# Performance work log

Hardware: AMD Instinct MI355X
Metric: run time of the kernel (lower is better)

## Reference

```python
import jax, jax.numpy as jnp
import numpy as np

NEG_SLOPE = 0.01  # torch F.leaky_relu default


def _gat_stack(x, W, a1w, a1b, a2w, a2b):
    """One GAT stack over all heads.
    x: (B, N, F_in); W: (H, F_in, d); a1w/a2w: (H, d); a1b/a2b: (H,)
    returns (B, N, H*d) -- heads concatenated in order along last dim.
    """
    # 1x1 conv1d (no bias) == per-node linear projection
    fts = jnp.einsum('bnf,hfd->hbnd', x, W)                      # (H,B,N,d)
    f1 = jnp.einsum('hbnd,hd->hbn', fts, a1w) + a1b[:, None, None]
    f2 = jnp.einsum('hbnd,hd->hbn', fts, a2w) + a2b[:, None, None]
    # logits[h,b,i,j] = f1[h,b,i] + f2[h,b,j]  (f_1.permute + f_2 broadcast)
    logits = f1[:, :, :, None] + f2[:, :, None, :]               # (H,B,N,N)
    coefs = jax.nn.softmax(jax.nn.leaky_relu(logits, NEG_SLOPE), axis=-1)
    vals = jnp.einsum('hbnm,hbmd->hbnd', coefs, fts)             # bmm aggregation
    ret = jax.nn.elu(vals + fts)                                 # residual-within-head + ELU activation
    B, N = x.shape[0], x.shape[1]
    return jnp.transpose(ret, (1, 2, 0, 3)).reshape(B, N, -1)    # cat(heads, dim=-1)


def setup_inputs() -> dict:
    key = jax.random.key(0)
    ks = jax.random.split(key, 7)
    B, N, F_in, H, d = 32, 512, 128, 8, 64
    hidden = H * d  # 512
    s = 0.05
    return {
        'x':   jax.random.normal(ks[0], (B, N, F_in), jnp.float32),
        'W0':  jax.random.normal(ks[1], (H, F_in, d), jnp.float32) * s,
        'W1':  jax.random.normal(ks[2], (H, hidden, d), jnp.float32) * s,
        'a1w': jax.random.normal(ks[3], (2, H, d), jnp.float32) * s,
        'a1b': jax.random.normal(ks[4], (2, H), jnp.float32) * s,
        'a2w': jax.random.normal(ks[5], (2, H, d), jnp.float32) * s,
        'a2b': jax.random.normal(ks[6], (2, H), jnp.float32) * s,
    }


def reference(x, W0, W1, a1w, a1b, a2w, a2b):
    # stack 0: input dim = num_random_sample
    h = _gat_stack(x, W0, a1w[0], a1b[0], a2w[0], a2b[0])
    # stack 1: input dim = hidden_dim
    out = _gat_stack(h, W1, a1w[1], a1b[1], a2w[1], a2b[1])
    return out
```

## Files before the change

### kernel.cpp

```cpp
#include <hip/hip_runtime.h>
#include <hip/hip_bf16.h>
#include <stdint.h>

typedef __attribute__((ext_vector_type(8))) short short8;
typedef __attribute__((ext_vector_type(4))) float f32x4;

#define L2E 1.44269504f
#define FN  131072

__device__ __forceinline__ short f2bf(float f) {
    unsigned u = __builtin_bit_cast(unsigned, f);
    return (short)((u + 0x8000u) >> 16);
}
__device__ __forceinline__ short f2bf_rn(float f) {
    __hip_bfloat16 h = __float2bfloat16(f);
    return __builtin_bit_cast(short, h);
}
__device__ __forceinline__ float bf2f(short s) {
    unsigned u = ((unsigned)(unsigned short)s) << 16;
    return __builtin_bit_cast(float, u);
}

__device__ __forceinline__ void gld16(void* l, const void* g) {
    __builtin_amdgcn_global_load_lds(
        (const __attribute__((address_space(1))) unsigned*)g,
        (__attribute__((address_space(3))) unsigned*)l, 16, 0, 0);
}

#define PIPE_OPEN()  do { __builtin_amdgcn_s_barrier();                        \
                          __builtin_amdgcn_sched_barrier(0);                   \
                          asm volatile("" ::: "memory"); } while (0)
#define PIPE_CLOSE() do { asm volatile("s_waitcnt lgkmcnt(0)" ::: "memory");   \
                          __builtin_amdgcn_sched_barrier(0);                   \
                          __builtin_amdgcn_s_barrier(); } while (0)

__global__ void wtrans_kernel(const float* __restrict__ W0, const float* __restrict__ W1,
                              short* __restrict__ BT0, short* __restrict__ BT1) {
    int idx = blockIdx.x * 256 + threadIdx.x;
    if (idx < 8 * 128 * 64) {
        int h = idx >> 13;
        int k = (idx >> 6) & 127;
        int dd = idx & 63;
        BT0[(h * 64 + dd) * 128 + k] = f2bf(W0[idx]);
    } else {
        int j = idx - 8 * 128 * 64;
        int h = j >> 15;
        int k = (j >> 6) & 511;
        int dd = j & 63;
        BT1[(h * 64 + dd) * 512 + k] = f2bf(W1[j]);
    }
}

template <typename AT>
__global__ __launch_bounds__(256, 2)
void gemm_kernel(const AT* __restrict__ A, const short* __restrict__ BT,
                 short* __restrict__ fts, int K,
                 const float* __restrict__ a1w, const float* __restrict__ a1b,
                 const float* __restrict__ a2w, const float* __restrict__ a2b,
                 float* __restrict__ fbuf) {
    __shared__ __align__(16) short As[2][128 * 64];
    __shared__ __align__(16) short Bs[2][128 * 64];

    const int tid  = threadIdx.x;
    const int lane = tid & 63;
    const int w    = tid >> 6;
    const int wr   = w >> 1, wc = w & 1;
    const int quad = lane >> 4, l15 = lane & 15;

    const int id = blockIdx.x;
    const int bx = (id >> 3) & 3;
    const int by = ((id >> 5) << 3) + (id & 7);
    const int m0 = by * 128;
    const int n0 = bx * 128;

    const int rl   = lane >> 3;
    const int cpos = lane & 7;
    const int kcl  = cpos ^ rl;

    f32x4 acc[4][4];
    for (int i = 0; i < 4; ++i)
        for (int j = 0; j < 4; ++j) { f32x4 z = {0.f, 0.f, 0.f, 0.f}; acc[i][j] = z; }

    const int nkb = K >> 6;

    if constexpr (sizeof(AT) == 4) {
        for (int kb = 0; kb < nkb; ++kb) {
            __syncthreads();
            for (int i = 0; i < 8; ++i) {
                int id2 = tid + i * 256;
                int row = id2 >> 4, q = id2 & 15;
                int c = q >> 1, half = q & 1;
                float4 v = *(const float4*)((const float*)A + (size_t)(m0 + row) * K + kb * 64 + q * 4);
                ushort4 p;
                p.x = (unsigned short)f2bf(v.x);
                p.y = (unsigned short)f2bf(v.y);
                p.z = (unsigned short)f2bf(v.z);
                p.w = (unsigned short)f2bf(v.w);
                int swz = c ^ (row & 7);
                *(ushort4*)(As[0] + row * 64 + swz * 8 + half * 4) = p;
            }
            for (int i = 0; i < 4; ++i) {
                int rowb = w * 32 + i * 8;
                gld16(Bs[0] + rowb * 64,
                      BT + (size_t)(n0 + rowb + rl) * K + kb * 64 + kcl * 8);
            }
            __syncthreads();
            short8 af[2][4], bf[2][4];
            for (int ks = 0; ks < 2; ++ks) {
                for (int mf = 0; mf < 4; ++mf) {
                    int row = wr * 64 + mf * 16 + l15;
                    af[ks][mf] = *(const short8*)(As[0] + row * 64 + (((ks * 4 + quad) ^ (row & 7)) << 3));
                }
                for (int nf = 0; nf < 4; ++nf) {
                    int row = wc * 64 + nf * 16 + l15;
                    bf[ks][nf] = *(const short8*)(Bs[0] + row * 64 + (((ks * 4 + quad) ^ (row & 7)) << 3));
                }
            }
            for (int ks = 0; ks < 2; ++ks)
                for (int mf = 0; mf < 4; ++mf)
                    for (int nf = 0; nf < 4; ++nf)
                        acc[mf][nf] = __builtin_amdgcn_mfma_f32_16x16x32_bf16(af[ks][mf], bf[ks][nf], acc[mf][nf], 0, 0, 0);
        }
    } else {
        auto stageAB = [&](int kb, int bufi) {
#pragma unroll
            for (int i = 0; i < 4; ++i) {
                int rowb = w * 32 + i * 8;
                gld16(As[bufi] + rowb * 64,
                      (const short*)A + (size_t)(m0 + rowb + rl) * K + kb * 64 + kcl * 8);
            }
#pragma unroll
            for (int i = 0; i < 4; ++i) {
                int rowb = w * 32 + i * 8;
                gld16(Bs[bufi] + rowb * 64,
                      BT + (size_t)(n0 + rowb + rl) * K + kb * 64 + kcl * 8);
            }
        };
        stageAB(0, 0);
        if (nkb > 1) stageAB(1, 1);
        for (int kb = 0; kb < nkb; ++kb) {
            if (kb + 1 < nkb) asm volatile("s_waitcnt vmcnt(8)" ::: "memory");
            else              asm volatile("s_waitcnt vmcnt(0)" ::: "memory");
            PIPE_OPEN();
            const short* as = As[kb & 1];
            const short* bs = Bs[kb & 1];
            short8 af[2][4], bf[2][4];
            for (int ks = 0; ks < 2; ++ks) {
                for (int mf = 0; mf < 4; ++mf) {
                    int row = wr * 64 + mf * 16 + l15;
                    af[ks][mf] = *(const short8*)(as + row * 64 + (((ks * 4 + quad) ^ (row & 7)) << 3));
                }
                for (int nf = 0; nf < 4; ++nf) {
                    int row = wc * 64 + nf * 16 + l15;
                    bf[ks][nf] = *(const short8*)(bs + row * 64 + (((ks * 4 + quad) ^ (row & 7)) << 3));
                }
            }
            for (int ks = 0; ks < 2; ++ks)
                for (int mf = 0; mf < 4; ++mf)
                    for (int nf = 0; nf < 4; ++nf)
                        acc[mf][nf] = __builtin_amdgcn_mfma_f32_16x16x32_bf16(af[ks][mf], bf[ks][nf], acc[mf][nf], 0, 0, 0);
            PIPE_CLOSE();
            if (kb + 2 < nkb) stageAB(kb + 2, kb & 1);
        }
    }

    for (int nf = 0; nf < 4; ++nf) {
        int col = n0 + wc * 64 + nf * 16 + l15;
        int h = col >> 6, dd = col & 63;
        for (int mf = 0; mf < 4; ++mf) {
            int m = m0 + wr * 64 + mf * 16 + quad * 4;
            int b = m >> 9, n = m & 511;
            ushort4 pk;
            pk.x = (unsigned short)f2bf(acc[mf][nf][0]);
            pk.y = (unsigned short)f2bf(acc[mf][nf][1]);
            pk.z = (unsigned short)f2bf(acc[mf][nf][2]);
            pk.w = (unsigned short)f2bf(acc[mf][nf][3]);
            *(ushort4*)(fts + (size_t)((h * 32 + b) * 64 + dd) * 512 + n) = pk;
        }
    }

    {
        const int head = (n0 >> 6) + wc;
        float w1[4], w2[4];
        for (int nf = 0; nf < 4; ++nf) {
            w1[nf] = a1w[head * 64 + nf * 16 + l15];
            w2[nf] = a2w[head * 64 + nf * 16 + l15];
        }
        const float b1 = a1b[head], b2 = a2b[head];
        const int rsel = l15 & 3;
        for (int mf = 0; mf < 4; ++mf) {
            float g1[4], g2[4];
            for (int r = 0; r < 4; ++r) {
                float s1 = 0.f, s2 = 0.f;
                for (int nf = 0; nf < 4; ++nf) {
                    s1 += acc[mf][nf][r] * w1[nf];
                    s2 += acc[mf][nf][r] * w2[nf];
                }
                for (int m = 1; m < 16; m <<= 1) {
                    s1 += __shfl_xor(s1, m, 64);
                    s2 += __shfl_xor(s2, m, 64);
                }
                g1[r] = s1; g2[r] = s2;
            }
            float v1 = rsel == 0 ? g1[0] : rsel == 1 ? g1[1] : rsel == 2 ? g1[2] : g1[3];
            float v2 = rsel == 0 ? g2[0] : rsel == 1 ? g2[1] : rsel == 2 ? g2[2] : g2[3];
            if (l15 < 4) {
                int m = m0 + wr * 64 + mf * 16 + quad * 4 + rsel;
                int b = m >> 9, i = m & 511;
                int fi = (head * 32 + b) * 512 + i;
                float f1 = v1 + b1, f2 = v2 + b2;
                fbuf[0 * FN + fi] = __builtin_amdgcn_exp2f(f1 * L2E);
                fbuf[1 * FN + fi] = __builtin_amdgcn_exp2f(f1 * (0.01f * L2E));
                fbuf[2 * FN + fi] = __builtin_amdgcn_exp2f(f2 * L2E);
                fbuf[3 * FN + fi] = __builtin_amdgcn_exp2f(f2 * (0.01f * L2E));
            }
        }
    }
}

template <typename OutT>
__global__ __launch_bounds__(256, 4)
void attn_kernel(const short* __restrict__ fts, const float* __restrict__ fbuf,
                 OutT* __restrict__ out) {
    __shared__ __align__(16) short fbs[4][64 * 64];
    __shared__ __align__(16) float p2_s[512];
    __shared__ __align__(16) float q2_s[512];

    const int tid  = threadIdx.x;
    const int lane = tid & 63, w = tid >> 6;
    const int quad = lane >> 4, l15 = lane & 15;
    const int bx   = blockIdx.x;
    const int quarter = bx >> 8;
    const int slab = bx & 255;
    const int h    = slab >> 5;
    const int b    = slab & 31;
    const int r0   = quarter * 128;
    const size_t fbase = (size_t)(slab * 64) * 512;
    const int fidx = slab * 512;

    const int srow = lane >> 3;
    const int spc  = lane & 7;

    f32x4 acc[2][4], accL[2];
    for (int i = 0; i < 2; ++i) {
        f32x4 z = {0.f, 0.f, 0.f, 0.f};
        accL[i] = z;
        for (int j = 0; j < 4; ++j) acc[i][j] = z;
    }
    short8 onesv;
    for (int t = 0; t < 8; ++t) onesv[t] = (short)0x3F80;

    float Rr[2];
    for (int rt = 0; rt < 2; ++rt) {
        int i = fidx + r0 + w * 32 + rt * 16 + l15;
        float P1 = fbuf[i];
        float Q1 = fbuf[1 * FN + i];
        Rr[rt] = Q1 * __builtin_amdgcn_rcpf(P1);
    }

    const float* p2g = fbuf + 2 * FN + fidx;
    const float* q2g = fbuf + 3 * FN + fidx;

    if (w < 2) gld16(p2_s + w * 256, p2g + w * 256 + lane * 4);
    else       gld16(q2_s + (w - 2) * 256, q2g + (w - 2) * 256 + lane * 4);

    auto stage = [&](int tc, short* buf) {
#pragma unroll
        for (int i = 0; i < 2; ++i) {
            int d0 = w * 16 + i * 8;
            int d  = d0 + srow;
            gld16(buf + d0 * 64,
                  fts + fbase + (size_t)d * 512 + tc * 64 + ((spc ^ srow) << 3));
        }
    };
    stage(0, fbs[0]);
    stage(1, fbs[1]);
    stage(2, fbs[2]);
    stage(3, fbs[3]);

#pragma unroll
    for (int tc = 0; tc < 8; ++tc) {
        if      (tc <= 4) asm volatile("s_waitcnt vmcnt(6)" ::: "memory");
        else if (tc == 5) asm volatile("s_waitcnt vmcnt(4)" ::: "memory");
        else if (tc == 6) asm volatile("s_waitcnt vmcnt(2)" ::: "memory");
        else              asm volatile("s_waitcnt vmcnt(0)" ::: "memory");
        PIPE_OPEN();

        short* buf = fbs[tc & 3];
#pragma unroll
        for (int jb = 0; jb < 2; ++jb) {
            short8 bfr[4];
#pragma unroll
            for (int nf = 0; nf < 4; ++nf) {
                int col = nf * 16 + l15;
                bfr[nf] = *(const short8*)(buf + col * 64 + (((jb * 4 + quad) ^ (col & 7)) << 3));
            }
            int o = tc * 64 + jb * 32 + quad * 8;
            f32x4 pa = *(const f32x4*)(p2_s + o), pb = *(const f32x4*)(p2_s + o + 4);
            f32x4 qa = *(const f32x4*)(q2_s + o), qb = *(const f32x4*)(q2_s + o + 4);
            float p2v[8] = {pa[0], pa[1], pa[2], pa[3], pb[0], pb[1], pb[2], pb[3]};
            float q2v[8] = {qa[0], qa[1], qa[2], qa[3], qb[0], qb[1], qb[2], qb[3]};

#pragma unroll
            for (int rt = 0; rt < 2; ++rt) {
                const float R = Rr[rt];
                short8 ef;
#pragma unroll
                for (int t = 0; t < 8; ++t)
                    ef[t] = f2bf_rn(fmaxf(p2v[t], R * q2v[t]));
                for (int nf = 0; nf < 4; ++nf)
                    acc[rt][nf] = __builtin_amdgcn_mfma_f32_16x16x32_bf16(ef, bfr[nf], acc[rt][nf], 0, 0, 0);
                accL[rt] = __builtin_amdgcn_mfma_f32_16x16x32_bf16(ef, onesv, accL[rt], 0, 0, 0);
            }
        }

        PIPE_CLOSE();
        if (tc + 4 < 8) stage(tc + 4, fbs[tc & 3]);
    }

    for (int rt = 0; rt < 2; ++rt) {
        float rinv[4];
        for (int r = 0; r < 4; ++r) rinv[r] = __builtin_amdgcn_rcpf(accL[rt][r]);
        int i0 = r0 + w * 32 + rt * 16 + quad * 4;
        for (int nf = 0; nf < 4; ++nf) {
            int col = nf * 16 + l15;
            ushort4 res = *(const ushort4*)(fts + fbase + col * 512 + i0);
            unsigned short rr[4] = {res.x, res.y, res.z, res.w};
            for (int r = 0; r < 4; ++r) {
                float val = acc[rt][nf][r] * rinv[r] + bf2f((short)rr[r]);
                if (val < 0.f) val = __builtin_amdgcn_exp2f(val * L2E) - 1.f;
                size_t oidx = (size_t)(b * 512 + i0 + r) * 512 + h * 64 + col;
                if constexpr (sizeof(OutT) == 4) out[oidx] = val;
                else                             out[oidx] = f2bf(val);
            }
        }
    }
}

extern "C" void kernel_launch(void* const* d_in, const int* in_sizes, int n_in,
                              void* d_out, int out_size, void* d_ws, size_t ws_size,
                              hipStream_t stream) {
    const float* x   = (const float*)d_in[0];
    const float* W0  = (const float*)d_in[1];
    const float* W1  = (const float*)d_in[2];
    const float* a1w = (const float*)d_in[3];
    const float* a1b = (const float*)d_in[4];
    const float* a2w = (const float*)d_in[5];
    const float* a2b = (const float*)d_in[6];
    float* out = (float*)d_out;

    char* ws = (char*)d_ws;
    short* BT0  = (short*)(ws);
    short* BT1  = (short*)(ws + 131072);
    float* fbuf = (float*)(ws + 655360);
    short* fts  = (short*)(ws + 2752512);
    short* hbuf = (short*)d_out;

    wtrans_kernel<<<1280, 256, 0, stream>>>(W0, W1, BT0, BT1);

    gemm_kernel<float><<<512, 256, 0, stream>>>(x, BT0, fts, 128,
                                                a1w, a1b, a2w, a2b, fbuf);
    attn_kernel<short><<<1024, 256, 0, stream>>>(fts, fbuf, hbuf);

    gemm_kernel<short><<<512, 256, 0, stream>>>(hbuf, BT1, fts, 512,
                                                a1w + 512, a1b + 8, a2w + 512, a2b + 8, fbuf);
    attn_kernel<float><<<1024, 256, 0, stream>>>(fts, fbuf, out);
}
```

Baseline: 144.7 us.

## Load full fts slab into LDS once and process 256 rows per block

The attention kernel now stages all eight 64-column chunks of the per-(head,batch) feature slab into LDS up front and waits once, instead of a four-deep rolling buffer. Each block handles half of the rows (256) rather than a quarter, so blocks drop from 1024 to 512 and each wave holds twice the accumulators. The residual term is read from LDS instead of global memory. This halves the redundant global loads of fts across blocks, but LDS use doubles, occupancy is lowered to 2 blocks per CU, and load latency is no longer overlapped with MFMA work.

```diff
diff --git a/kernel.cpp b/kernel.cpp
--- a/kernel.cpp
+++ b/kernel.cpp
@@ -219,10 +219,10 @@
 }
 
 template <typename OutT>
-__global__ __launch_bounds__(256, 4)
+__global__ __launch_bounds__(256, 2)
 void attn_kernel(const short* __restrict__ fts, const float* __restrict__ fbuf,
                  OutT* __restrict__ out) {
-    __shared__ __align__(16) short fbs[4][64 * 64];
+    __shared__ __align__(16) short fts_s[8][64 * 64];
     __shared__ __align__(16) float p2_s[512];
     __shared__ __align__(16) float q2_s[512];
 
@@ -230,19 +230,20 @@
     const int lane = tid & 63, w = tid >> 6;
     const int quad = lane >> 4, l15 = lane & 15;
     const int bx   = blockIdx.x;
-    const int quarter = bx >> 8;
+    const int half = bx >> 8;
     const int slab = bx & 255;
     const int h    = slab >> 5;
     const int b    = slab & 31;
-    const int r0   = quarter * 128;
+    const int r0   = half * 256;
     const size_t fbase = (size_t)(slab * 64) * 512;
     const int fidx = slab * 512;
 
     const int srow = lane >> 3;
     const int spc  = lane & 7;
 
-    f32x4 acc[2][4], accL[2];
-    for (int i = 0; i < 2; ++i) {
+    f32x4 acc[4][4], accL[4];
+#pragma unroll
+    for (int i = 0; i < 4; ++i) {
         f32x4 z = {0.f, 0.f, 0.f, 0.f};
         accL[i] = z;
         for (int j = 0; j < 4; ++j) acc[i][j] = z;
@@ -250,9 +251,10 @@
     short8 onesv;
     for (int t = 0; t < 8; ++t) onesv[t] = (short)0x3F80;
 
-    float Rr[2];
-    for (int rt = 0; rt < 2; ++rt) {
-        int i = fidx + r0 + w * 32 + rt * 16 + l15;
+    float Rr[4];
+#pragma unroll
+    for (int rt = 0; rt < 4; ++rt) {
+        int i = fidx + r0 + w * 64 + rt * 16 + l15;
         float P1 = fbuf[i];
         float Q1 = fbuf[1 * FN + i];
         Rr[rt] = Q1 * __builtin_amdgcn_rcpf(P1);
@@ -264,29 +266,23 @@
     if (w < 2) gld16(p2_s + w * 256, p2g + w * 256 + lane * 4);
     else       gld16(q2_s + (w - 2) * 256, q2g + (w - 2) * 256 + lane * 4);
 
-    auto stage = [&](int tc, short* buf) {
+#pragma unroll
+    for (int tc = 0; tc < 8; ++tc) {
 #pragma unroll
         for (int i = 0; i < 2; ++i) {
             int d0 = w * 16 + i * 8;
             int d  = d0 + srow;
-            gld16(buf + d0 * 64,
+            gld16(&fts_s[tc][0] + d0 * 64,
                   fts + fbase + (size_t)d * 512 + tc * 64 + ((spc ^ srow) << 3));
         }
-    };
-    stage(0, fbs[0]);
-    stage(1, fbs[1]);
-    stage(2, fbs[2]);
-    stage(3, fbs[3]);
+    }
+
+    asm volatile("s_waitcnt vmcnt(0)" ::: "memory");
+    PIPE_OPEN();
 
 #pragma unroll
     for (int tc = 0; tc < 8; ++tc) {
-        if      (tc <= 4) asm volatile("s_waitcnt vmcnt(6)" ::: "memory");
-        else if (tc == 5) asm volatile("s_waitcnt vmcnt(4)" ::: "memory");
-        else if (tc == 6) asm volatile("s_waitcnt vmcnt(2)" ::: "memory");
-        else              asm volatile("s_waitcnt vmcnt(0)" ::: "memory");
-        PIPE_OPEN();
-
-        short* buf = fbs[tc & 3];
+        const short* buf = &fts_s[tc][0];
 #pragma unroll
         for (int jb = 0; jb < 2; ++jb) {
             short8 bfr[4];
@@ -302,7 +298,7 @@
             float q2v[8] = {qa[0], qa[1], qa[2], qa[3], qb[0], qb[1], qb[2], qb[3]};
 
 #pragma unroll
-            for (int rt = 0; rt < 2; ++rt) {
+            for (int rt = 0; rt < 4; ++rt) {
                 const float R = Rr[rt];
                 short8 ef;
 #pragma unroll
@@ -313,18 +309,20 @@
                 accL[rt] = __builtin_amdgcn_mfma_f32_16x16x32_bf16(ef, onesv, accL[rt], 0, 0, 0);
             }
         }
-
-        PIPE_CLOSE();
-        if (tc + 4 < 8) stage(tc + 4, fbs[tc & 3]);
-    }
-
-    for (int rt = 0; rt < 2; ++rt) {
+    }
+
+#pragma unroll
+    for (int rt = 0; rt < 4; ++rt) {
         float rinv[4];
         for (int r = 0; r < 4; ++r) rinv[r] = __builtin_amdgcn_rcpf(accL[rt][r]);
-        int i0 = r0 + w * 32 + rt * 16 + quad * 4;
+        int i0 = r0 + w * 64 + rt * 16 + quad * 4;
+        int nn = i0 & 511;
+        int tcC = nn >> 6, nl = nn & 63;
+#pragma unroll
         for (int nf = 0; nf < 4; ++nf) {
             int col = nf * 16 + l15;
-            ushort4 res = *(const ushort4*)(fts + fbase + col * 512 + i0);
+            const short* rbase = &fts_s[tcC][0] + col * 64 + (((nl >> 3) ^ (col & 7)) << 3) + (nl & 7);
+            ushort4 res = *(const ushort4*)rbase;
             unsigned short rr[4] = {res.x, res.y, res.z, res.w};
             for (int r = 0; r < 4; ++r) {
                 float val = acc[rt][nf][r] * rinv[r] + bf2f((short)rr[r]);
@@ -360,9 +358,9 @@
 
     gemm_kernel<float><<<512, 256, 0, stream>>>(x, BT0, fts, 128,
                                                 a1w, a1b, a2w, a2b, fbuf);
-    attn_kernel<short><<<1024, 256, 0, stream>>>(fts, fbuf, hbuf);
+    attn_kernel<short><<<512, 256, 0, stream>>>(fts, fbuf, hbuf);
 
     gemm_kernel<short><<<512, 256, 0, stream>>>(hbuf, BT1, fts, 512,
                                                 a1w + 512, a1b + 8, a2w + 512, a2b + 8, fbuf);
-    attn_kernel<float><<<1024, 256, 0, stream>>>(fts, fbuf, out);
-}
+    attn_kernel<float><<<512, 256, 0, stream>>>(fts, fbuf, out);
+}
```

New measurement: 146.4 us. Within noise of the previous version (+1.2%).
